# Kernel tuning notes

Measured on AMD Instinct MI355X. Metric: run time of the kernel, lower is better.

Reference implementation:

```python
import jax, jax.numpy as jnp
import numpy as np

B, S, D_IN, D_OUT = 4, 2048, 1024, 1024

def setup_inputs() -> dict:
    key = jax.random.key(0)
    ks = jax.random.split(key, 6)
    s = 1.0 / np.sqrt(D_IN)
    return {
        "inputs": jax.random.normal(ks[0], (B, S, D_IN), dtype=jnp.float32),
        "Wq": jax.random.normal(ks[1], (D_IN, D_OUT), dtype=jnp.float32) * s,
        "Wk": jax.random.normal(ks[2], (D_IN, D_OUT), dtype=jnp.float32) * s,
        "Wv": jax.random.normal(ks[3], (D_IN, D_OUT), dtype=jnp.float32) * s,
        "Wo": jax.random.normal(ks[4], (D_OUT, D_OUT), dtype=jnp.float32) * (1.0 / np.sqrt(D_OUT)),
        "bo": jax.random.normal(ks[5], (D_OUT,), dtype=jnp.float32) * 0.01,
    }

def reference(inputs, Wq, Wk, Wv, Wo, bo):
    # QKV projections (no bias, matching qkv_bias=False)
    q = inputs @ Wq  # [B,S,D]
    k = inputs @ Wk
    v = inputs @ Wv
    # naive full attention: scores [B,S,S]
    scores = jnp.einsum('bqd,bkd->bqk', q, k) / jnp.sqrt(jnp.asarray(k.shape[-1], q.dtype))
    attn = jax.nn.softmax(scores, axis=-1)
    out = jnp.einsum('bqk,bkd->bqd', attn, v)
    return out @ Wo + bo
```

## Files before the change

kernel.cpp:

```cpp
#include <hip/hip_runtime.h>
#include <hip/hip_bf16.h>
#include <cstdint>

typedef __attribute__((ext_vector_type(8))) __bf16 bf16x8;
typedef __attribute__((ext_vector_type(4))) float  f32x4;

__device__ __forceinline__ unsigned short f2bf(float x) {
    union { float f; unsigned u; } v; v.f = x;
    unsigned r = v.u + 0x7fffu + ((v.u >> 16) & 1u);
    return (unsigned short)(r >> 16);
}
__device__ __forceinline__ unsigned pack2bf(float a, float b) {
    return (unsigned)f2bf(a) | ((unsigned)f2bf(b) << 16);
}

__device__ __forceinline__ void gld_lds16(const unsigned short* g, unsigned short* l) {
    __builtin_amdgcn_global_load_lds(
        (const __attribute__((address_space(1))) unsigned int*)g,
        (__attribute__((address_space(3))) unsigned int*)l,
        16, 0, 0);
}

__global__ void cvt_kernel(const float* __restrict__ in, unsigned short* __restrict__ out, int n4) {
    int i = blockIdx.x * blockDim.x + threadIdx.x;
    if (i < n4) {
        float4 f = ((const float4*)in)[i];
        ushort4 o;
        o.x = f2bf(f.x); o.y = f2bf(f.y); o.z = f2bf(f.z); o.w = f2bf(f.w);
        ((ushort4*)out)[i] = o;
    }
}

__global__ void wtrans_kernel(const float* __restrict__ W, unsigned short* __restrict__ out) {
    __shared__ float tile[32][33];
    int bx = blockIdx.x, by = blockIdx.y;
    int tx = threadIdx.x, ty = threadIdx.y;
#pragma unroll
    for (int j = 0; j < 4; j++)
        tile[ty + j*8][tx] = W[(size_t)(bx*32 + ty + j*8) * 1024 + by*32 + tx];
    __syncthreads();
#pragma unroll
    for (int j = 0; j < 4; j++)
        out[(size_t)(by*32 + ty + j*8) * 1024 + bx*32 + tx] = f2bf(tile[tx][ty + j*8]);
}

__global__ void vtrans_kernel(const unsigned short* __restrict__ qkv, unsigned short* __restrict__ vt) {
    __shared__ unsigned short tile[32][33];
    int b = blockIdx.z;
    const unsigned short* V = qkv + (size_t)b * 2048 * 3072 + 2048;
    unsigned short* out = vt + (size_t)b * 1024 * 2048;
    int bx = blockIdx.x, by = blockIdx.y;
    int tx = threadIdx.x, ty = threadIdx.y;
#pragma unroll
    for (int j = 0; j < 4; j++)
        tile[ty + j*8][tx] = V[(size_t)(bx*32 + ty + j*8) * 3072 + by*32 + tx];
    __syncthreads();
#pragma unroll
    for (int j = 0; j < 4; j++)
        out[(size_t)(by*32 + ty + j*8) * 2048 + bx*32 + tx] = tile[tx][ty + j*8];
}

__global__ void softmax_kernel(unsigned short* __restrict__ S) {
    const size_t row = blockIdx.x;
    unsigned short* p = S + row * 2048;
    const int tid = threadIdx.x;
    const int wave = tid >> 6, lane = tid & 63;

    uint4 raw = ((const uint4*)p)[tid];
    unsigned u[4] = {raw.x, raw.y, raw.z, raw.w};
    float x[8];
#pragma unroll
    for (int i = 0; i < 4; i++) {
        x[2*i]   = __uint_as_float(u[i] << 16);
        x[2*i+1] = __uint_as_float(u[i] & 0xffff0000u);
    }
    float m = x[0];
#pragma unroll
    for (int i = 1; i < 8; i++) m = fmaxf(m, x[i]);
#pragma unroll
    for (int off = 32; off >= 1; off >>= 1) m = fmaxf(m, __shfl_xor(m, off, 64));
    __shared__ float sm[4], ss[4];
    if (lane == 0) sm[wave] = m;
    __syncthreads();
    m = fmaxf(fmaxf(sm[0], sm[1]), fmaxf(sm[2], sm[3]));

    float e[8], s = 0.f;
#pragma unroll
    for (int i = 0; i < 8; i++) { e[i] = __expf(x[i] - m); s += e[i]; }
#pragma unroll
    for (int off = 32; off >= 1; off >>= 1) s += __shfl_xor(s, off, 64);
    if (lane == 0) ss[wave] = s;
    __syncthreads();
    s = ss[0] + ss[1] + ss[2] + ss[3];
    float inv = 1.0f / s;

    unsigned o[4];
#pragma unroll
    for (int i = 0; i < 4; i++)
        o[i] = pack2bf(e[2*i] * inv, e[2*i+1] * inv);
    ((uint4*)p)[tid] = make_uint4(o[0], o[1], o[2], o[3]);
}

template<bool OUT_BF16, bool BIAS>
__global__ __launch_bounds__(256)
void gemm_nt(const unsigned short* __restrict__ A, const unsigned short* __restrict__ B,
             void* __restrict__ C, const float* __restrict__ bias,
             int lda, int ldb, int ldc, int nk2, float scale,
             long long sA, long long sB, long long sC)
{
    __shared__ __align__(16) char smem[32768];
    unsigned short* As = (unsigned short*)smem;
    unsigned short* Bs = (unsigned short*)(smem + 16384);

    const int tid  = threadIdx.x;
    const int lane = tid & 63;
    const int wave = tid >> 6;
    const int bz = blockIdx.z;
    A += (size_t)bz * sA;
    B += (size_t)bz * sB;
    const int bm = blockIdx.y * 128;
    const int bn = blockIdx.x * 128;

    const int srow = tid >> 2;
    const int scol = ((tid & 3) ^ ((tid >> 3) & 3)) * 8;

    const unsigned short* pa0 = A + (size_t)(bm + srow) * lda + scol;
    const unsigned short* pa1 = pa0 + 32;
    const unsigned short* pa2 = A + (size_t)(bm + 64 + srow) * lda + scol;
    const unsigned short* pa3 = pa2 + 32;
    const unsigned short* pb0 = B + (size_t)(bn + srow) * ldb + scol;
    const unsigned short* pb1 = pb0 + 32;
    const unsigned short* pb2 = B + (size_t)(bn + 64 + srow) * ldb + scol;
    const unsigned short* pb3 = pb2 + 32;

    f32x4 acc[4][4];
#pragma unroll
    for (int i = 0; i < 4; i++)
#pragma unroll
        for (int j = 0; j < 4; j++) acc[i][j] = (f32x4){0.f, 0.f, 0.f, 0.f};

    const int wm = (wave & 1) * 64;
    const int wn = (wave >> 1) * 64;
    const int ln15 = lane & 15;
    const int quad = lane >> 4;
    const int fko = (quad ^ ((ln15 >> 1) & 3)) * 8;

    const int ldsoff = tid * 16;

    for (int kt = 0; kt < nk2; ++kt) {
        __syncthreads();
        gld_lds16(pa0, (unsigned short*)(smem         + ldsoff));
        gld_lds16(pa2, (unsigned short*)(smem + 4096  + ldsoff));
        gld_lds16(pa1, (unsigned short*)(smem + 8192  + ldsoff));
        gld_lds16(pa3, (unsigned short*)(smem + 12288 + ldsoff));
        gld_lds16(pb0, (unsigned short*)(smem + 16384 + ldsoff));
        gld_lds16(pb2, (unsigned short*)(smem + 20480 + ldsoff));
        gld_lds16(pb1, (unsigned short*)(smem + 24576 + ldsoff));
        gld_lds16(pb3, (unsigned short*)(smem + 28672 + ldsoff));
        pa0 += 64; pa1 += 64; pa2 += 64; pa3 += 64;
        pb0 += 64; pb1 += 64; pb2 += 64; pb3 += 64;
        asm volatile("s_waitcnt vmcnt(0)" ::: "memory");
        __syncthreads();

#pragma unroll
        for (int t = 0; t < 2; t++) {
            bf16x8 af[4], bfr[4];
#pragma unroll
            for (int i = 0; i < 4; i++)
                af[i] = *(const bf16x8*)&As[t*4096 + (wm + i*16 + ln15) * 32 + fko];
#pragma unroll
            for (int j = 0; j < 4; j++)
                bfr[j] = *(const bf16x8*)&Bs[t*4096 + (wn + j*16 + ln15) * 32 + fko];
#pragma unroll
            for (int i = 0; i < 4; i++)
#pragma unroll
                for (int j = 0; j < 4; j++)
                    acc[i][j] = __builtin_amdgcn_mfma_f32_16x16x32_bf16(af[i], bfr[j], acc[i][j], 0, 0, 0);
        }
    }

    if (OUT_BF16) {
        __syncthreads();
        float* ep = (float*)(smem + wave * 4352);
        unsigned short* Co = (unsigned short*)C + (size_t)bz * sC;
#pragma unroll
        for (int i = 0; i < 4; i++) {
#pragma unroll
            for (int j = 0; j < 4; j++) {
#pragma unroll
                for (int r = 0; r < 4; r++)
                    ep[(quad*4 + r) * 68 + j*16 + ln15] = acc[i][j][r] * scale;
            }
            __builtin_amdgcn_s_waitcnt(0);
#pragma unroll
            for (int p = 0; p < 2; p++) {
                int lrow = p*8 + (lane >> 3);
                int col0 = (lane & 7) * 8;
                float4 lo = *(const float4*)&ep[lrow * 68 + col0];
                float4 hi = *(const float4*)&ep[lrow * 68 + col0 + 4];
                uint4 o;
                o.x = pack2bf(lo.x, lo.y);
                o.y = pack2bf(lo.z, lo.w);
                o.z = pack2bf(hi.x, hi.y);
                o.w = pack2bf(hi.z, hi.w);
                *(uint4*)&Co[(size_t)(bm + wm + i*16 + lrow) * ldc + bn + wn + col0] = o;
            }
            __builtin_amdgcn_s_waitcnt(0);
        }
    } else {
        float bval[4];
        if (BIAS) {
#pragma unroll
            for (int j = 0; j < 4; j++) bval[j] = bias[bn + wn + j*16 + ln15];
        }
        float* Co = (float*)C + (size_t)bz * sC;
#pragma unroll
        for (int i = 0; i < 4; i++) {
            int r0 = bm + wm + i*16 + quad*4;
#pragma unroll
            for (int j = 0; j < 4; j++) {
                int c = bn + wn + j*16 + ln15;
#pragma unroll
                for (int r = 0; r < 4; r++) {
                    float v = acc[i][j][r] * scale;
                    Co[(size_t)(r0 + r) * ldc + c] = v + (BIAS ? bval[j] : 0.f);
                }
            }
        }
    }
}

extern "C" void kernel_launch(void* const* d_in, const int* in_sizes, int n_in,
                              void* d_out, int out_size, void* d_ws, size_t ws_size,
                              hipStream_t stream) {
    const float* X  = (const float*)d_in[0];
    const float* Wq = (const float*)d_in[1];
    const float* Wk = (const float*)d_in[2];
    const float* Wv = (const float*)d_in[3];
    const float* Wo = (const float*)d_in[4];
    const float* bo = (const float*)d_in[5];
    float* out = (float*)d_out;

    size_t off = 0;
    auto alloc = [&](size_t bytes) {
        void* p = (char*)d_ws + off;
        off += (bytes + 255) & ~(size_t)255;
        return p;
    };
    unsigned short* Xbf  = (unsigned short*)alloc(8192ull * 1024 * 2);
    unsigned short* Wcat = (unsigned short*)alloc(3072ull * 1024 * 2);
    unsigned short* WoT  = (unsigned short*)alloc(1024ull * 1024 * 2);
    unsigned short* QKV  = (unsigned short*)alloc(8192ull * 3072 * 2);
    unsigned short* VT   = (unsigned short*)alloc(4ull * 1024 * 2048 * 2);
    unsigned short* Sc   = (unsigned short*)alloc(4ull * 2048 * 2048 * 2);
    unsigned short* AO   = Xbf;

    cvt_kernel<<<(8192*1024/4 + 255)/256, 256, 0, stream>>>(X, Xbf, 8192*1024/4);
    dim3 tb(32, 8);
    wtrans_kernel<<<dim3(32,32), tb, 0, stream>>>(Wq, Wcat);
    wtrans_kernel<<<dim3(32,32), tb, 0, stream>>>(Wk, Wcat + 1024*1024);
    wtrans_kernel<<<dim3(32,32), tb, 0, stream>>>(Wv, Wcat + 2*1024*1024);
    wtrans_kernel<<<dim3(32,32), tb, 0, stream>>>(Wo, WoT);

    gemm_nt<true,false><<<dim3(3072/128, 8192/128, 1), 256, 0, stream>>>(
        Xbf, Wcat, QKV, nullptr, 1024, 1024, 3072, 16, 1.0f, 0, 0, 0);

    vtrans_kernel<<<dim3(64, 32, 4), tb, 0, stream>>>(QKV, VT);

    gemm_nt<true,false><<<dim3(2048/128, 2048/128, 4), 256, 0, stream>>>(
        QKV, QKV + 1024, Sc, nullptr, 3072, 3072, 2048, 16, 0.03125f,
        2048ll*3072, 2048ll*3072, 2048ll*2048);

    softmax_kernel<<<8192, 256, 0, stream>>>(Sc);

    gemm_nt<true,false><<<dim3(1024/128, 2048/128, 4), 256, 0, stream>>>(
        Sc, VT, AO, nullptr, 2048, 2048, 1024, 32, 1.0f,
        2048ll*2048, 1024ll*2048, 2048ll*1024);

    gemm_nt<false,true><<<dim3(1024/128, 8192/128, 1), 256, 0, stream>>>(
        AO, WoT, out, bo, 1024, 1024, 1024, 16, 1.0f, 0, 0, 0);

    (void)n_in; (void)in_sizes; (void)out_size; (void)ws_size;
}
```

Before: 309.4 us.

## Pre-pack B operands into MFMA fragment layout and load directly to registers

Weights, K and V are written in a packed per-fragment layout, so each lane loads its MFMA B operand with a single 16-byte global load instead of staging B through LDS. The QKV GEMM epilogue writes Q row-major and K/V directly in packed form, which removes the separate V transpose kernel and halves LDS usage per block. The trade-off is more global loads per thread in the main loop without any LDS reuse of B across waves, and a more complex multi-region epilogue.

New measurement: 308.5 us. About the same (-0.3%).

```diff
diff --git a/kernel.cpp b/kernel.cpp
--- a/kernel.cpp
+++ b/kernel.cpp
@@ -31,33 +31,18 @@
     }
 }
 
-__global__ void wtrans_kernel(const float* __restrict__ W, unsigned short* __restrict__ out) {
-    __shared__ float tile[32][33];
-    int bx = blockIdx.x, by = blockIdx.y;
-    int tx = threadIdx.x, ty = threadIdx.y;
-#pragma unroll
-    for (int j = 0; j < 4; j++)
-        tile[ty + j*8][tx] = W[(size_t)(bx*32 + ty + j*8) * 1024 + by*32 + tx];
-    __syncthreads();
-#pragma unroll
-    for (int j = 0; j < 4; j++)
-        out[(size_t)(by*32 + ty + j*8) * 1024 + bx*32 + tx] = f2bf(tile[tx][ty + j*8]);
-}
-
-__global__ void vtrans_kernel(const unsigned short* __restrict__ qkv, unsigned short* __restrict__ vt) {
-    __shared__ unsigned short tile[32][33];
-    int b = blockIdx.z;
-    const unsigned short* V = qkv + (size_t)b * 2048 * 3072 + 2048;
-    unsigned short* out = vt + (size_t)b * 1024 * 2048;
-    int bx = blockIdx.x, by = blockIdx.y;
-    int tx = threadIdx.x, ty = threadIdx.y;
-#pragma unroll
-    for (int j = 0; j < 4; j++)
-        tile[ty + j*8][tx] = V[(size_t)(bx*32 + ty + j*8) * 3072 + by*32 + tx];
-    __syncthreads();
-#pragma unroll
-    for (int j = 0; j < 4; j++)
-        out[(size_t)(by*32 + ty + j*8) * 2048 + bx*32 + tx] = tile[tx][ty + j*8];
+__global__ void wpack_kernel(const float* __restrict__ W, unsigned short* __restrict__ out) {
+    int tid  = threadIdx.x;
+    int lane = tid & 63;
+    int chunk = blockIdx.x * 4 + (tid >> 6);
+    int nt = chunk >> 5, k32 = chunk & 31;
+    int r = lane & 15, q = lane >> 4;
+    const float* src = W + (size_t)(k32*32 + q*8) * 1024 + nt*16 + r;
+    unsigned o[4];
+#pragma unroll
+    for (int i = 0; i < 4; i++)
+        o[i] = pack2bf(src[(size_t)(2*i) * 1024], src[(size_t)(2*i+1) * 1024]);
+    *(uint4*)(out + (size_t)chunk * 512 + lane * 8) = make_uint4(o[0], o[1], o[2], o[3]);
 }
 
 __global__ void softmax_kernel(unsigned short* __restrict__ S) {
@@ -101,43 +86,33 @@
     ((uint4*)p)[tid] = make_uint4(o[0], o[1], o[2], o[3]);
 }
 
-template<bool OUT_BF16, bool BIAS>
+template<int EPI>
 __global__ __launch_bounds__(256)
-void gemm_nt(const unsigned short* __restrict__ A, const unsigned short* __restrict__ B,
-             void* __restrict__ C, const float* __restrict__ bias,
-             int lda, int ldb, int ldc, int nk2, float scale,
+void gemm_pk(const unsigned short* __restrict__ A, const unsigned short* __restrict__ Bpk,
+             void* __restrict__ C, unsigned short* __restrict__ Ck, unsigned short* __restrict__ Cv,
+             const float* __restrict__ bias,
+             int lda, int ldc, int KS, int nk2, float scale,
              long long sA, long long sB, long long sC)
 {
-    __shared__ __align__(16) char smem[32768];
+    constexpr int SMEM = (EPI == 2) ? 34816 : ((EPI == 1) ? 17408 : 16384);
+    __shared__ __align__(16) char smem[SMEM];
     unsigned short* As = (unsigned short*)smem;
-    unsigned short* Bs = (unsigned short*)(smem + 16384);
 
     const int tid  = threadIdx.x;
     const int lane = tid & 63;
     const int wave = tid >> 6;
     const int bz = blockIdx.z;
-    A += (size_t)bz * sA;
-    B += (size_t)bz * sB;
+    A   += (size_t)bz * sA;
+    Bpk += (size_t)bz * sB;
     const int bm = blockIdx.y * 128;
     const int bn = blockIdx.x * 128;
 
     const int srow = tid >> 2;
     const int scol = ((tid & 3) ^ ((tid >> 3) & 3)) * 8;
-
     const unsigned short* pa0 = A + (size_t)(bm + srow) * lda + scol;
     const unsigned short* pa1 = pa0 + 32;
     const unsigned short* pa2 = A + (size_t)(bm + 64 + srow) * lda + scol;
     const unsigned short* pa3 = pa2 + 32;
-    const unsigned short* pb0 = B + (size_t)(bn + srow) * ldb + scol;
-    const unsigned short* pb1 = pb0 + 32;
-    const unsigned short* pb2 = B + (size_t)(bn + 64 + srow) * ldb + scol;
-    const unsigned short* pb3 = pb2 + 32;
-
-    f32x4 acc[4][4];
-#pragma unroll
-    for (int i = 0; i < 4; i++)
-#pragma unroll
-        for (int j = 0; j < 4; j++) acc[i][j] = (f32x4){0.f, 0.f, 0.f, 0.f};
 
     const int wm = (wave & 1) * 64;
     const int wn = (wave >> 1) * 64;
@@ -145,52 +120,78 @@
     const int quad = lane >> 4;
     const int fko = (quad ^ ((ln15 >> 1) & 3)) * 8;
 
+    const unsigned short* pb[4];
+#pragma unroll
+    for (int j = 0; j < 4; j++)
+        pb[j] = Bpk + (size_t)(((bn + wn + j*16) >> 4) * KS) * 512 + lane * 8;
+
+    f32x4 acc[4][4];
+#pragma unroll
+    for (int i = 0; i < 4; i++)
+#pragma unroll
+        for (int j = 0; j < 4; j++) acc[i][j] = (f32x4){0.f, 0.f, 0.f, 0.f};
+
     const int ldsoff = tid * 16;
 
     for (int kt = 0; kt < nk2; ++kt) {
         __syncthreads();
-        gld_lds16(pa0, (unsigned short*)(smem         + ldsoff));
+        gld_lds16(pa0, (unsigned short*)(smem + ldsoff));
         gld_lds16(pa2, (unsigned short*)(smem + 4096  + ldsoff));
         gld_lds16(pa1, (unsigned short*)(smem + 8192  + ldsoff));
         gld_lds16(pa3, (unsigned short*)(smem + 12288 + ldsoff));
-        gld_lds16(pb0, (unsigned short*)(smem + 16384 + ldsoff));
-        gld_lds16(pb2, (unsigned short*)(smem + 20480 + ldsoff));
-        gld_lds16(pb1, (unsigned short*)(smem + 24576 + ldsoff));
-        gld_lds16(pb3, (unsigned short*)(smem + 28672 + ldsoff));
         pa0 += 64; pa1 += 64; pa2 += 64; pa3 += 64;
-        pb0 += 64; pb1 += 64; pb2 += 64; pb3 += 64;
+        bf16x8 b0[4], b1[4];
+#pragma unroll
+        for (int j = 0; j < 4; j++) {
+            b0[j] = *(const bf16x8*)(pb[j]);
+            b1[j] = *(const bf16x8*)(pb[j] + 512);
+            pb[j] += 1024;
+        }
         asm volatile("s_waitcnt vmcnt(0)" ::: "memory");
         __syncthreads();
 
 #pragma unroll
         for (int t = 0; t < 2; t++) {
-            bf16x8 af[4], bfr[4];
+            bf16x8 af[4];
 #pragma unroll
             for (int i = 0; i < 4; i++)
                 af[i] = *(const bf16x8*)&As[t*4096 + (wm + i*16 + ln15) * 32 + fko];
 #pragma unroll
-            for (int j = 0; j < 4; j++)
-                bfr[j] = *(const bf16x8*)&Bs[t*4096 + (wn + j*16 + ln15) * 32 + fko];
-#pragma unroll
             for (int i = 0; i < 4; i++)
 #pragma unroll
                 for (int j = 0; j < 4; j++)
-                    acc[i][j] = __builtin_amdgcn_mfma_f32_16x16x32_bf16(af[i], bfr[j], acc[i][j], 0, 0, 0);
+                    acc[i][j] = __builtin_amdgcn_mfma_f32_16x16x32_bf16(
+                        af[i], t ? b1[j] : b0[j], acc[i][j], 0, 0, 0);
         }
     }
 
-    if (OUT_BF16) {
+    if (EPI == 0) {
+        float bval[4];
+#pragma unroll
+        for (int j = 0; j < 4; j++) bval[j] = bias[bn + wn + j*16 + ln15];
+        float* Co = (float*)C + (size_t)bz * sC;
+#pragma unroll
+        for (int i = 0; i < 4; i++) {
+            int r0 = bm + wm + i*16 + quad*4;
+#pragma unroll
+            for (int j = 0; j < 4; j++) {
+                int c = bn + wn + j*16 + ln15;
+#pragma unroll
+                for (int r = 0; r < 4; r++)
+                    Co[(size_t)(r0 + r) * ldc + c] = acc[i][j][r] * scale + bval[j];
+            }
+        }
+    } else if (EPI == 1) {
         __syncthreads();
         float* ep = (float*)(smem + wave * 4352);
         unsigned short* Co = (unsigned short*)C + (size_t)bz * sC;
 #pragma unroll
         for (int i = 0; i < 4; i++) {
 #pragma unroll
-            for (int j = 0; j < 4; j++) {
+            for (int j = 0; j < 4; j++)
 #pragma unroll
                 for (int r = 0; r < 4; r++)
                     ep[(quad*4 + r) * 68 + j*16 + ln15] = acc[i][j][r] * scale;
-            }
             __builtin_amdgcn_s_waitcnt(0);
 #pragma unroll
             for (int p = 0; p < 2; p++) {
@@ -199,33 +200,71 @@
                 float4 lo = *(const float4*)&ep[lrow * 68 + col0];
                 float4 hi = *(const float4*)&ep[lrow * 68 + col0 + 4];
                 uint4 o;
-                o.x = pack2bf(lo.x, lo.y);
-                o.y = pack2bf(lo.z, lo.w);
-                o.z = pack2bf(hi.x, hi.y);
-                o.w = pack2bf(hi.z, hi.w);
+                o.x = pack2bf(lo.x, lo.y); o.y = pack2bf(lo.z, lo.w);
+                o.z = pack2bf(hi.x, hi.y); o.w = pack2bf(hi.z, hi.w);
                 *(uint4*)&Co[(size_t)(bm + wm + i*16 + lrow) * ldc + bn + wn + col0] = o;
             }
             __builtin_amdgcn_s_waitcnt(0);
         }
     } else {
-        float bval[4];
-        if (BIAS) {
-#pragma unroll
-            for (int j = 0; j < 4; j++) bval[j] = bias[bn + wn + j*16 + ln15];
-        }
-        float* Co = (float*)C + (size_t)bz * sC;
-#pragma unroll
-        for (int i = 0; i < 4; i++) {
-            int r0 = bm + wm + i*16 + quad*4;
-#pragma unroll
-            for (int j = 0; j < 4; j++) {
-                int c = bn + wn + j*16 + ln15;
-#pragma unroll
-                for (int r = 0; r < 4; r++) {
-                    float v = acc[i][j][r] * scale;
-                    Co[(size_t)(r0 + r) * ldc + c] = v + (BIAS ? bval[j] : 0.f);
+        __syncthreads();
+        float* ep = (float*)(smem + wave * 8704);
+        const int region = bn >> 10;
+#pragma unroll
+        for (int half = 0; half < 2; half++) {
+#pragma unroll
+            for (int ii = 0; ii < 2; ii++) {
+                int i = half*2 + ii;
+#pragma unroll
+                for (int j = 0; j < 4; j++)
+#pragma unroll
+                    for (int r = 0; r < 4; r++)
+                        ep[(ii*16 + quad*4 + r) * 68 + j*16 + ln15] = acc[i][j][r] * scale;
+            }
+            __builtin_amdgcn_s_waitcnt(0);
+            const int mrow0 = bm + wm + half*32;
+            if (region == 0) {
+                unsigned short* Q = (unsigned short*)C;
+#pragma unroll
+                for (int p = 0; p < 4; p++) {
+                    int lrow = p*8 + (lane >> 3);
+                    int col0 = (lane & 7) * 8;
+                    float4 lo = *(const float4*)&ep[lrow * 68 + col0];
+                    float4 hi = *(const float4*)&ep[lrow * 68 + col0 + 4];
+                    uint4 o;
+                    o.x = pack2bf(lo.x, lo.y); o.y = pack2bf(lo.z, lo.w);
+                    o.z = pack2bf(hi.x, hi.y); o.w = pack2bf(hi.z, hi.w);
+                    *(uint4*)&Q[(size_t)(mrow0 + lrow) * ldc + bn + wn + col0] = o;
+                }
+            } else if (region == 1) {
+#pragma unroll
+                for (int mt = 0; mt < 2; mt++)
+#pragma unroll
+                    for (int c = 0; c < 2; c++) {
+                        float4 f0 = *(const float4*)&ep[(mt*16 + ln15) * 68 + c*32 + quad*8];
+                        float4 f1 = *(const float4*)&ep[(mt*16 + ln15) * 68 + c*32 + quad*8 + 4];
+                        uint4 o;
+                        o.x = pack2bf(f0.x, f0.y); o.y = pack2bf(f0.z, f0.w);
+                        o.z = pack2bf(f1.x, f1.y); o.w = pack2bf(f1.z, f1.w);
+                        int cid = ((mrow0 + mt*16) >> 4) * 32 + ((bn - 1024 + wn + c*32) >> 5);
+                        *(uint4*)(Ck + (size_t)cid * 512 + lane * 8) = o;
+                    }
+            } else {
+                int s32 = mrow0 >> 5;
+#pragma unroll
+                for (int dt = 0; dt < 4; dt++) {
+                    float v[8];
+#pragma unroll
+                    for (int e = 0; e < 8; e++)
+                        v[e] = ep[(quad*8 + e) * 68 + dt*16 + ln15];
+                    uint4 o;
+                    o.x = pack2bf(v[0], v[1]); o.y = pack2bf(v[2], v[3]);
+                    o.z = pack2bf(v[4], v[5]); o.w = pack2bf(v[6], v[7]);
+                    int cid = (((bn - 2048 + wn) >> 4) + dt) * 256 + s32;
+                    *(uint4*)(Cv + (size_t)cid * 512 + lane * 8) = o;
                 }
             }
+            __builtin_amdgcn_s_waitcnt(0);
         }
     }
 }
@@ -248,37 +287,35 @@
         return p;
     };
     unsigned short* Xbf  = (unsigned short*)alloc(8192ull * 1024 * 2);
-    unsigned short* Wcat = (unsigned short*)alloc(3072ull * 1024 * 2);
-    unsigned short* WoT  = (unsigned short*)alloc(1024ull * 1024 * 2);
-    unsigned short* QKV  = (unsigned short*)alloc(8192ull * 3072 * 2);
-    unsigned short* VT   = (unsigned short*)alloc(4ull * 1024 * 2048 * 2);
+    unsigned short* Wpk  = (unsigned short*)alloc(192ull * 32 * 512 * 2);
+    unsigned short* Wopk = (unsigned short*)alloc(64ull * 32 * 512 * 2);
+    unsigned short* Qrm  = (unsigned short*)alloc(8192ull * 1024 * 2);
+    unsigned short* Kpk  = (unsigned short*)alloc(512ull * 32 * 512 * 2);
+    unsigned short* Vpk  = (unsigned short*)alloc(64ull * 256 * 512 * 2);
     unsigned short* Sc   = (unsigned short*)alloc(4ull * 2048 * 2048 * 2);
     unsigned short* AO   = Xbf;
 
     cvt_kernel<<<(8192*1024/4 + 255)/256, 256, 0, stream>>>(X, Xbf, 8192*1024/4);
-    dim3 tb(32, 8);
-    wtrans_kernel<<<dim3(32,32), tb, 0, stream>>>(Wq, Wcat);
-    wtrans_kernel<<<dim3(32,32), tb, 0, stream>>>(Wk, Wcat + 1024*1024);
-    wtrans_kernel<<<dim3(32,32), tb, 0, stream>>>(Wv, Wcat + 2*1024*1024);
-    wtrans_kernel<<<dim3(32,32), tb, 0, stream>>>(Wo, WoT);
-
-    gemm_nt<true,false><<<dim3(3072/128, 8192/128, 1), 256, 0, stream>>>(
-        Xbf, Wcat, QKV, nullptr, 1024, 1024, 3072, 16, 1.0f, 0, 0, 0);
-
-    vtrans_kernel<<<dim3(64, 32, 4), tb, 0, stream>>>(QKV, VT);
-
-    gemm_nt<true,false><<<dim3(2048/128, 2048/128, 4), 256, 0, stream>>>(
-        QKV, QKV + 1024, Sc, nullptr, 3072, 3072, 2048, 16, 0.03125f,
-        2048ll*3072, 2048ll*3072, 2048ll*2048);
+    wpack_kernel<<<512, 256, 0, stream>>>(Wq, Wpk);
+    wpack_kernel<<<512, 256, 0, stream>>>(Wk, Wpk + 64*32*512);
+    wpack_kernel<<<512, 256, 0, stream>>>(Wv, Wpk + 128*32*512);
+    wpack_kernel<<<512, 256, 0, stream>>>(Wo, Wopk);
+
+    gemm_pk<2><<<dim3(3072/128, 8192/128, 1), 256, 0, stream>>>(
+        Xbf, Wpk, Qrm, Kpk, Vpk, nullptr, 1024, 1024, 32, 16, 1.0f, 0, 0, 0);
+
+    gemm_pk<1><<<dim3(2048/128, 2048/128, 4), 256, 0, stream>>>(
+        Qrm, Kpk, Sc, nullptr, nullptr, nullptr, 1024, 2048, 32, 16, 0.03125f,
+        2048ll*1024, 128ll*32*512, 2048ll*2048);
 
     softmax_kernel<<<8192, 256, 0, stream>>>(Sc);
 
-    gemm_nt<true,false><<<dim3(1024/128, 2048/128, 4), 256, 0, stream>>>(
-        Sc, VT, AO, nullptr, 2048, 2048, 1024, 32, 1.0f,
-        2048ll*2048, 1024ll*2048, 2048ll*1024);
-
-    gemm_nt<false,true><<<dim3(1024/128, 8192/128, 1), 256, 0, stream>>>(
-        AO, WoT, out, bo, 1024, 1024, 1024, 16, 1.0f, 0, 0, 0);
+    gemm_pk<1><<<dim3(1024/128, 2048/128, 4), 256, 0, stream>>>(
+        Sc, Vpk, AO, nullptr, nullptr, nullptr, 2048, 1024, 256, 32, 1.0f,
+        2048ll*2048, 64ll*512, 2048ll*1024);
+
+    gemm_pk<0><<<dim3(1024/128, 8192/128, 1), 256, 0, stream>>>(
+        AO, Wopk, out, nullptr, nullptr, bo, 1024, 1024, 32, 16, 1.0f, 0, 0, 0);
 
     (void)n_in; (void)in_sizes; (void)out_size; (void)ws_size;
 }
```

## Fuse V transpose into QKV GEMM epilogue and stage fp32 output through LDS

Applied to the files above, without the earlier changes.

The QKV projection epilogue now writes Q and K into separate row-major buffers and writes V already transposed into the VT layout, which removes the separate V-transpose kernel and its extra read and write of V. The output projection epilogue now stages fp32 results through LDS and writes coalesced float4 rows with bias, replacing scattered scalar stores. The transposed V stores are 32-byte column-wise chunks per lane, so that write pattern is less coalesced than the row-major paths.

New measurement: 315.4 us. Within noise of the previous version (+1.9%).

```diff
diff --git a/kernel.cpp b/kernel.cpp
--- a/kernel.cpp
+++ b/kernel.cpp
@@ -44,22 +44,6 @@
         out[(size_t)(by*32 + ty + j*8) * 1024 + bx*32 + tx] = f2bf(tile[tx][ty + j*8]);
 }
 
-__global__ void vtrans_kernel(const unsigned short* __restrict__ qkv, unsigned short* __restrict__ vt) {
-    __shared__ unsigned short tile[32][33];
-    int b = blockIdx.z;
-    const unsigned short* V = qkv + (size_t)b * 2048 * 3072 + 2048;
-    unsigned short* out = vt + (size_t)b * 1024 * 2048;
-    int bx = blockIdx.x, by = blockIdx.y;
-    int tx = threadIdx.x, ty = threadIdx.y;
-#pragma unroll
-    for (int j = 0; j < 4; j++)
-        tile[ty + j*8][tx] = V[(size_t)(bx*32 + ty + j*8) * 3072 + by*32 + tx];
-    __syncthreads();
-#pragma unroll
-    for (int j = 0; j < 4; j++)
-        out[(size_t)(by*32 + ty + j*8) * 2048 + bx*32 + tx] = tile[tx][ty + j*8];
-}
-
 __global__ void softmax_kernel(unsigned short* __restrict__ S) {
     const size_t row = blockIdx.x;
     unsigned short* p = S + row * 2048;
@@ -101,10 +85,11 @@
     ((uint4*)p)[tid] = make_uint4(o[0], o[1], o[2], o[3]);
 }
 
-template<bool OUT_BF16, bool BIAS>
+template<int EPI>
 __global__ __launch_bounds__(256)
 void gemm_nt(const unsigned short* __restrict__ A, const unsigned short* __restrict__ B,
-             void* __restrict__ C, const float* __restrict__ bias,
+             void* __restrict__ C, unsigned short* __restrict__ CK, unsigned short* __restrict__ CV,
+             const float* __restrict__ bias,
              int lda, int ldb, int ldc, int nk2, float scale,
              long long sA, long long sB, long long sC)
 {
@@ -123,7 +108,6 @@
 
     const int srow = tid >> 2;
     const int scol = ((tid & 3) ^ ((tid >> 3) & 3)) * 8;
-
     const unsigned short* pa0 = A + (size_t)(bm + srow) * lda + scol;
     const unsigned short* pa1 = pa0 + 32;
     const unsigned short* pa2 = A + (size_t)(bm + 64 + srow) * lda + scol;
@@ -144,7 +128,6 @@
     const int ln15 = lane & 15;
     const int quad = lane >> 4;
     const int fko = (quad ^ ((ln15 >> 1) & 3)) * 8;
-
     const int ldsoff = tid * 16;
 
     for (int kt = 0; kt < nk2; ++kt) {
@@ -179,18 +162,45 @@
         }
     }
 
-    if (OUT_BF16) {
-        __syncthreads();
-        float* ep = (float*)(smem + wave * 4352);
-        unsigned short* Co = (unsigned short*)C + (size_t)bz * sC;
+    __syncthreads();
+    float* ep = (float*)(smem + wave * 4352);
+
+    if (EPI == 0) {
+        float* Co = (float*)C + (size_t)bz * sC;
+        const float* bp = bias + bn + wn;
 #pragma unroll
         for (int i = 0; i < 4; i++) {
 #pragma unroll
-            for (int j = 0; j < 4; j++) {
+            for (int j = 0; j < 4; j++)
 #pragma unroll
                 for (int r = 0; r < 4; r++)
                     ep[(quad*4 + r) * 68 + j*16 + ln15] = acc[i][j][r] * scale;
+            __builtin_amdgcn_s_waitcnt(0);
+#pragma unroll
+            for (int p = 0; p < 2; p++) {
+                int lrow = p*8 + (lane >> 3);
+                int col0 = (lane & 7) * 8;
+                float4 lo = *(const float4*)&ep[lrow * 68 + col0];
+                float4 hi = *(const float4*)&ep[lrow * 68 + col0 + 4];
+                float4 b0 = *(const float4*)&bp[col0];
+                float4 b1 = *(const float4*)&bp[col0 + 4];
+                lo.x += b0.x; lo.y += b0.y; lo.z += b0.z; lo.w += b0.w;
+                hi.x += b1.x; hi.y += b1.y; hi.z += b1.z; hi.w += b1.w;
+                float* dst = &Co[(size_t)(bm + wm + i*16 + lrow) * ldc + bn + wn + col0];
+                *(float4*)dst = lo;
+                *(float4*)(dst + 4) = hi;
             }
+            __builtin_amdgcn_s_waitcnt(0);
+        }
+    } else if (EPI == 1) {
+        unsigned short* Co = (unsigned short*)C + (size_t)bz * sC;
+#pragma unroll
+        for (int i = 0; i < 4; i++) {
+#pragma unroll
+            for (int j = 0; j < 4; j++)
+#pragma unroll
+                for (int r = 0; r < 4; r++)
+                    ep[(quad*4 + r) * 68 + j*16 + ln15] = acc[i][j][r] * scale;
             __builtin_amdgcn_s_waitcnt(0);
 #pragma unroll
             for (int p = 0; p < 2; p++) {
@@ -199,33 +209,51 @@
                 float4 lo = *(const float4*)&ep[lrow * 68 + col0];
                 float4 hi = *(const float4*)&ep[lrow * 68 + col0 + 4];
                 uint4 o;
-                o.x = pack2bf(lo.x, lo.y);
-                o.y = pack2bf(lo.z, lo.w);
-                o.z = pack2bf(hi.x, hi.y);
-                o.w = pack2bf(hi.z, hi.w);
+                o.x = pack2bf(lo.x, lo.y); o.y = pack2bf(lo.z, lo.w);
+                o.z = pack2bf(hi.x, hi.y); o.w = pack2bf(hi.z, hi.w);
                 *(uint4*)&Co[(size_t)(bm + wm + i*16 + lrow) * ldc + bn + wn + col0] = o;
             }
             __builtin_amdgcn_s_waitcnt(0);
         }
     } else {
-        float bval[4];
-        if (BIAS) {
-#pragma unroll
-            for (int j = 0; j < 4; j++) bval[j] = bias[bn + wn + j*16 + ln15];
-        }
-        float* Co = (float*)C + (size_t)bz * sC;
+        const int region = bn >> 10;
+        const int b = bm >> 11;
 #pragma unroll
         for (int i = 0; i < 4; i++) {
-            int r0 = bm + wm + i*16 + quad*4;
-#pragma unroll
-            for (int j = 0; j < 4; j++) {
-                int c = bn + wn + j*16 + ln15;
-#pragma unroll
-                for (int r = 0; r < 4; r++) {
-                    float v = acc[i][j][r] * scale;
-                    Co[(size_t)(r0 + r) * ldc + c] = v + (BIAS ? bval[j] : 0.f);
+#pragma unroll
+            for (int j = 0; j < 4; j++)
+#pragma unroll
+                for (int r = 0; r < 4; r++)
+                    ep[(quad*4 + r) * 68 + j*16 + ln15] = acc[i][j][r];
+            __builtin_amdgcn_s_waitcnt(0);
+            if (region < 2) {
+                unsigned short* Co = (region == 0) ? (unsigned short*)C : CK;
+                int cn = (bn & 1023) + wn;
+#pragma unroll
+                for (int p = 0; p < 2; p++) {
+                    int lrow = p*8 + (lane >> 3);
+                    int col0 = (lane & 7) * 8;
+                    float4 lo = *(const float4*)&ep[lrow * 68 + col0];
+                    float4 hi = *(const float4*)&ep[lrow * 68 + col0 + 4];
+                    uint4 o;
+                    o.x = pack2bf(lo.x, lo.y); o.y = pack2bf(lo.z, lo.w);
+                    o.z = pack2bf(hi.x, hi.y); o.w = pack2bf(hi.z, hi.w);
+                    *(uint4*)&Co[(size_t)(bm + wm + i*16 + lrow) * 1024 + cn + col0] = o;
                 }
+            } else {
+                float v[16];
+#pragma unroll
+                for (int r = 0; r < 16; r++) v[r] = ep[r * 68 + lane];
+                unsigned o[8];
+#pragma unroll
+                for (int t = 0; t < 8; t++) o[t] = pack2bf(v[2*t], v[2*t+1]);
+                int d = (bn - 2048) + wn + lane;
+                int s0 = (bm & 2047) + wm + i*16;
+                unsigned short* dst = CV + (size_t)b * 1024 * 2048 + (size_t)d * 2048 + s0;
+                *(uint4*)dst       = make_uint4(o[0], o[1], o[2], o[3]);
+                *(uint4*)(dst + 8) = make_uint4(o[4], o[5], o[6], o[7]);
             }
+            __builtin_amdgcn_s_waitcnt(0);
         }
     }
 }
@@ -250,7 +278,8 @@
     unsigned short* Xbf  = (unsigned short*)alloc(8192ull * 1024 * 2);
     unsigned short* Wcat = (unsigned short*)alloc(3072ull * 1024 * 2);
     unsigned short* WoT  = (unsigned short*)alloc(1024ull * 1024 * 2);
-    unsigned short* QKV  = (unsigned short*)alloc(8192ull * 3072 * 2);
+    unsigned short* Qrm  = (unsigned short*)alloc(8192ull * 1024 * 2);
+    unsigned short* Krm  = (unsigned short*)alloc(8192ull * 1024 * 2);
     unsigned short* VT   = (unsigned short*)alloc(4ull * 1024 * 2048 * 2);
     unsigned short* Sc   = (unsigned short*)alloc(4ull * 2048 * 2048 * 2);
     unsigned short* AO   = Xbf;
@@ -262,23 +291,21 @@
     wtrans_kernel<<<dim3(32,32), tb, 0, stream>>>(Wv, Wcat + 2*1024*1024);
     wtrans_kernel<<<dim3(32,32), tb, 0, stream>>>(Wo, WoT);
 
-    gemm_nt<true,false><<<dim3(3072/128, 8192/128, 1), 256, 0, stream>>>(
-        Xbf, Wcat, QKV, nullptr, 1024, 1024, 3072, 16, 1.0f, 0, 0, 0);
-
-    vtrans_kernel<<<dim3(64, 32, 4), tb, 0, stream>>>(QKV, VT);
-
-    gemm_nt<true,false><<<dim3(2048/128, 2048/128, 4), 256, 0, stream>>>(
-        QKV, QKV + 1024, Sc, nullptr, 3072, 3072, 2048, 16, 0.03125f,
-        2048ll*3072, 2048ll*3072, 2048ll*2048);
+    gemm_nt<2><<<dim3(3072/128, 8192/128, 1), 256, 0, stream>>>(
+        Xbf, Wcat, Qrm, Krm, VT, nullptr, 1024, 1024, 0, 16, 1.0f, 0, 0, 0);
+
+    gemm_nt<1><<<dim3(2048/128, 2048/128, 4), 256, 0, stream>>>(
+        Qrm, Krm, Sc, nullptr, nullptr, nullptr, 1024, 1024, 2048, 16, 0.03125f,
+        2048ll*1024, 2048ll*1024, 2048ll*2048);
 
     softmax_kernel<<<8192, 256, 0, stream>>>(Sc);
 
-    gemm_nt<true,false><<<dim3(1024/128, 2048/128, 4), 256, 0, stream>>>(
-        Sc, VT, AO, nullptr, 2048, 2048, 1024, 32, 1.0f,
+    gemm_nt<1><<<dim3(1024/128, 2048/128, 4), 256, 0, stream>>>(
+        Sc, VT, AO, nullptr, nullptr, nullptr, 2048, 2048, 1024, 32, 1.0f,
         2048ll*2048, 1024ll*2048, 2048ll*1024);
 
-    gemm_nt<false,true><<<dim3(1024/128, 8192/128, 1), 256, 0, stream>>>(
-        AO, WoT, out, bo, 1024, 1024, 1024, 16, 1.0f, 0, 0, 0);
+    gemm_nt<0><<<dim3(1024/128, 8192/128, 1), 256, 0, stream>>>(
+        AO, WoT, out, nullptr, nullptr, bo, 1024, 1024, 1024, 16, 1.0f, 0, 0, 0);
 
     (void)n_in; (void)in_sizes; (void)out_size; (void)ws_size;
 }
```
